# Optimization experiments

Hardware: AMD Instinct MI355X
Metric: run time of the kernel (lower is better)

Reference implementation:

```python
import jax, jax.numpy as jnp
import numpy as np

N = 100000
E = 1600000
NEG_SLOPE = 0.2


def _gat_layer(x, src, dst, W, a_src, a_dst, b, heads, out_ch):
    n = x.shape[0]
    h = (x @ W).reshape(n, heads, out_ch)                      # [N,H,C]
    alpha_src = (h * a_src).sum(-1)                            # [N,H]
    alpha_dst = (h * a_dst).sum(-1)                            # [N,H]
    e = jax.nn.leaky_relu(alpha_src[src] + alpha_dst[dst], NEG_SLOPE)  # [E,H]
    # segment softmax over incoming edges of each destination node
    m = jax.ops.segment_max(e, dst, num_segments=n)            # [N,H]
    ex = jnp.exp(e - m[dst])
    denom = jax.ops.segment_sum(ex, dst, num_segments=n)       # [N,H]
    alpha = ex / (denom[dst] + 1e-16)                          # [E,H]
    msg = h[src] * alpha[:, :, None]                           # [E,H,C]
    out = jax.ops.segment_sum(msg, dst, num_segments=n)        # [N,H,C]
    return out.reshape(n, heads * out_ch) + b


def setup_inputs() -> dict:
    key = jax.random.key(0)
    ks = jax.random.split(key, 10)
    glorot = lambda k, shape: jax.random.normal(k, shape, jnp.float32) * np.sqrt(2.0 / (shape[0] + shape[-1]))
    x = jax.random.normal(ks[0], (N, 5), jnp.float32)
    edge_index = jax.random.randint(ks[1], (2, E), 0, N, jnp.int64)
    return {
        "x": x,
        "edge_index": edge_index,
        "W1": glorot(ks[2], (5, 64)),
        "a_src1": glorot(ks[3], (8, 8)),
        "a_dst1": glorot(ks[4], (8, 8)),
        "b1": jnp.zeros((64,), jnp.float32),
        "W2": glorot(ks[5], (64, 2)),
        "a_src2": glorot(ks[6], (1, 2)),
        "a_dst2": glorot(ks[7], (1, 2)),
        "b2": jnp.zeros((2,), jnp.float32),
    }


def reference(x, edge_index, W1, a_src1, a_dst1, b1, W2, a_src2, a_dst2, b2):
    n = x.shape[0]
    loop = jnp.arange(n, dtype=edge_index.dtype)
    src = jnp.concatenate([edge_index[0], loop])   # PyG GATConv adds self-loops
    dst = jnp.concatenate([edge_index[1], loop])
    # dropout layers are no-ops in eval mode
    h = jax.nn.elu(_gat_layer(x, src, dst, W1, a_src1, a_dst1, b1, heads=8, out_ch=8))
    out = _gat_layer(h, src, dst, W2, a_src2, a_dst2, b2, heads=1, out_ch=2)
    return jax.nn.log_softmax(out, axis=1)
```

## Files before the change

kernel.cpp:

```cpp
#include <hip/hip_runtime.h>
#include <hip/hip_fp16.h>
#include <math.h>
#include <stdint.h>

#define N_NODES 100000
#define N_EDGES 1600000
#define N_TOT   (N_EDGES + N_NODES)
#define NEG_SLOPE 0.2f
#define LOG2E 1.44269504088896340736f

#define CB     128
#define CBBITS 7
#define NCB    ((N_NODES + CB - 1) / CB)
#define TP     2048
#define NPB    ((N_EDGES + TP - 1) / TP)
#define WINB   2560
#define NB_NODE1 ((N_NODES * 8 + 511) / 512)
#define N8     ((size_t)N_NODES * 8)

typedef int nt_int4 __attribute__((ext_vector_type(4)));

__global__ void __launch_bounds__(512) k_np(
        const int* __restrict__ src, const int* __restrict__ dst,
        int* __restrict__ ofsT, unsigned* __restrict__ pairs,
        const float* __restrict__ x, const float* __restrict__ W1,
        const float* __restrict__ a_src1, const float* __restrict__ a_dst1,
        __half* __restrict__ xh, __half* __restrict__ as1h,
        float* __restrict__ ad1) {
    __shared__ int lcnt[1024];
    __shared__ unsigned stage[TP];
    __shared__ int wred[8];
    int t = threadIdx.x;

    if (blockIdx.x >= NPB) {
        int gid  = (blockIdx.x - NPB) * 512 + t;
        int n    = gid >> 3;
        int head = gid & 7;
        if (n >= N_NODES) return;

        float xv[5];
#pragma unroll
        for (int k = 0; k < 5; ++k) xv[k] = x[n * 5 + k];

        float as = 0.f, ad = 0.f;
#pragma unroll
        for (int j = 0; j < 8; ++j) {
            int c = head * 8 + j;
            float acc = 0.f;
#pragma unroll
            for (int k = 0; k < 5; ++k) acc += xv[k] * W1[k * 64 + c];
            as += acc * a_src1[c];
            ad += acc * a_dst1[c];
        }
        as1h[n * 8 + head] = __float2half(as * LOG2E);
        ad1[n * 8 + head] = ad * LOG2E;

        if (head == 0) {
            __half2 p0 = __halves2half2(__float2half(xv[0]), __float2half(xv[1]));
            __half2 p1 = __halves2half2(__float2half(xv[2]), __float2half(xv[3]));
            __half2 p2 = __halves2half2(__float2half(xv[4]), __float2half(0.f));
            __half2 p3 = __halves2half2(__float2half(0.f), __float2half(0.f));
            __half2* xp = (__half2*)&xh[(size_t)n * 8];
            xp[0] = p0; xp[1] = p1; xp[2] = p2; xp[3] = p3;
        }
        return;
    }

    int blk = blockIdx.x;
    int base = blk * TP + t * 4;
    bool act = base < N_EDGES;
    int nE = min(TP, N_EDGES - blk * TP);

    lcnt[t] = 0; lcnt[t + 512] = 0;
    __syncthreads();

    nt_int4 s4, d4;
    if (act) {
        s4 = __builtin_nontemporal_load((const nt_int4*)(src + base));
        d4 = __builtin_nontemporal_load((const nt_int4*)(dst + base));
#pragma unroll
        for (int j = 0; j < 4; ++j) atomicAdd(&lcnt[d4[j] >> CBBITS], 1);
    }
    __syncthreads();

    int b0 = lcnt[t * 2], b1 = lcnt[t * 2 + 1];
    int local = b0 + b1;
    int ln = t & 63, w = t >> 6;
    int sc = local;
#pragma unroll
    for (int off = 1; off < 64; off <<= 1) {
        int u = __shfl_up(sc, off, 64);
        if (ln >= off) sc += u;
    }
    if (ln == 63) wred[w] = sc;
    __syncthreads();
    if (t < 8) {
        int v = wred[t], s = v;
#pragma unroll
        for (int off = 1; off < 8; off <<= 1) {
            int u = __shfl_up(s, off, 8);
            if ((t & 7) >= off) s += u;
        }
        wred[t] = s - v;
    }
    __syncthreads();
    int run = wred[w] + sc - local;
    lcnt[t * 2] = run; lcnt[t * 2 + 1] = run + b0;
    if (t * 2     <= NCB) ofsT[(size_t)(t * 2)     * NPB + blk] = run;
    if (t * 2 + 1 <= NCB) ofsT[(size_t)(t * 2 + 1) * NPB + blk] = run + b0;
    __syncthreads();

    if (act) {
#pragma unroll
        for (int j = 0; j < 4; ++j) {
            int d = d4[j], s = s4[j];
            int bin = d >> CBBITS;
            int idx = atomicAdd(&lcnt[bin], 1);
            stage[idx] = ((unsigned)(d & (CB - 1)) << 17) | (unsigned)s;
        }
    }
    __syncthreads();
    for (int i = t; i < nE; i += 512)
        pairs[(size_t)blk * TP + i] = stage[i];
}

__global__ void __launch_bounds__(512) k_csr(
        const int* __restrict__ ofsT, const unsigned* __restrict__ pairs,
        int* __restrict__ rbeg, int* __restrict__ rend, int* __restrict__ ssrc) {
    __shared__ unsigned stIn[WINB];
    __shared__ int stOut[WINB];
    __shared__ int lcnt[CB], lofs[CB], lcur[CB];
    __shared__ int wsum[2];
    __shared__ int acur;
    int B = blockIdx.x, t = threadIdx.x;
    int nvalid = min(CB, N_NODES - B * CB);
    int obase = B * WINB;

    if (t < CB) {
        lcnt[t] = (t < nvalid) ? 1 : 0;
        lcur[t] = 1;
    }
    if (t == 0) acur = 0;
    __syncthreads();

    for (int blk = t; blk < NPB; blk += 512) {
        int o0 = ofsT[(size_t)B       * NPB + blk];
        int o1 = ofsT[(size_t)(B + 1) * NPB + blk];
        int n = o1 - o0;
        if (n > 0) {
            int p = atomicAdd(&acur, n);
            const unsigned* pp = pairs + (size_t)blk * TP + o0;
            for (int i = 0; i < n; ++i) {
                unsigned r = pp[i];
                stIn[p + i] = r;
                atomicAdd(&lcnt[r >> 17], 1);
            }
        }
    }
    __syncthreads();
    int m = acur;

    int v = (t < CB) ? lcnt[t] : 0;
    int ln = t & 63, wv = t >> 6;
    int sc = v;
#pragma unroll
    for (int off = 1; off < 64; off <<= 1) {
        int u = __shfl_up(sc, off, 64);
        if (ln >= off) sc += u;
    }
    if (ln == 63 && wv < 2) wsum[wv] = sc;
    __syncthreads();
    int wbase = (wv == 1) ? wsum[0] : 0;
    int ex = wbase + sc - v;
    if (t < CB) {
        lofs[t] = ex;
        int gi = B * CB + t;
        if (gi < N_NODES) {
            rbeg[gi] = obase + ex;
            rend[gi] = obase + ex + v;
            stOut[ex] = gi;
        }
    }
    __syncthreads();

    for (int k = t; k < m; k += 512) {
        unsigned p = stIn[k];
        int dl = p >> 17;
        int idx = atomicAdd(&lcur[dl], 1);
        stOut[lofs[dl] + idx] = (int)(p & 0x1FFFF);
    }
    __syncthreads();

    int tot = m + nvalid;
    for (int i = t; i < tot; i += 512) ssrc[obase + i] = stOut[i];
}

__global__ void __launch_bounds__(256) k_gather1(
        const int* __restrict__ rbeg, const int* __restrict__ rend,
        const int* __restrict__ ssrc, const float4* __restrict__ xh4,
        const __half* __restrict__ as1h, const float* __restrict__ ad1,
        float* __restrict__ xsbuf) {
    int gtid = blockIdx.x * blockDim.x + threadIdx.x;
    int d      = gtid >> 5;
    int lane32 = threadIdx.x & 31;
    if (d >= N_NODES) return;
    int e = lane32 >> 3;
    int h = lane32 & 7;

    int beg = rbeg[d], end = rend[d];
    float adv = ad1[d * 8 + h];
    float c0 = 0.f, c1 = 0.f, c2 = 0.f, c3 = 0.f, c4 = 0.f, den = 0.f;

    for (int k = beg; k < end; k += 8) {
        int kA = k + e, kB = k + 4 + e;
        bool vA = kA < end, vB = kB < end;
        int sA = ssrc[vA ? kA : beg];
        int sB = ssrc[vB ? kB : beg];
        float eA = __half2float(as1h[sA * 8 + h]);
        float eB = __half2float(as1h[sB * 8 + h]);
        float4 xA = xh4[sA];
        float4 xB = xh4[sB];
        float tA = eA + adv; tA = fmaxf(tA, NEG_SLOPE * tA);
        float tB = eB + adv; tB = fmaxf(tB, NEG_SLOPE * tB);
        float wA = vA ? __builtin_amdgcn_exp2f(tA) : 0.f;
        float wB = vB ? __builtin_amdgcn_exp2f(tB) : 0.f;
        float2 A01 = __half22float2(*(__half2*)&xA.x);
        float2 A23 = __half22float2(*(__half2*)&xA.y);
        float2 A4_ = __half22float2(*(__half2*)&xA.z);
        float2 B01 = __half22float2(*(__half2*)&xB.x);
        float2 B23 = __half22float2(*(__half2*)&xB.y);
        float2 B4_ = __half22float2(*(__half2*)&xB.z);
        c0 += wA * A01.x + wB * B01.x;
        c1 += wA * A01.y + wB * B01.y;
        c2 += wA * A23.x + wB * B23.x;
        c3 += wA * A23.y + wB * B23.y;
        c4 += wA * A4_.x + wB * B4_.x;
        den += wA + wB;
    }

#define REDH(x) x += __shfl_xor(x, 8, 64); x += __shfl_xor(x, 16, 64);
    REDH(c0) REDH(c1) REDH(c2) REDH(c3) REDH(c4) REDH(den)
#undef REDH

    if (e == 0) {
        float inv = 1.f / den;
        size_t idx = (size_t)d * 8 + h;
        xsbuf[idx]          = c0 * inv;
        xsbuf[N8 + idx]     = c1 * inv;
        xsbuf[2 * N8 + idx] = c2 * inv;
        xsbuf[3 * N8 + idx] = c3 * inv;
        xsbuf[4 * N8 + idx] = c4 * inv;
    }
}

__global__ void __launch_bounds__(256) k_rec(
        const float* __restrict__ xsbuf, const float* __restrict__ b1,
        const float* __restrict__ W1, const float* __restrict__ W2,
        const float* __restrict__ a_src2, const float* __restrict__ a_dst2,
        float4* __restrict__ rec) {
    int gtid = blockIdx.x * blockDim.x + threadIdx.x;
    int d = gtid >> 3;
    int h = gtid & 7;
    if (d >= N_NODES) return;

    size_t idx = (size_t)d * 8 + h;
    float xs[5] = { xsbuf[idx], xsbuf[N8 + idx], xsbuf[2 * N8 + idx],
                    xsbuf[3 * N8 + idx], xsbuf[4 * N8 + idx] };

    float4 hA = ((const float4*)b1)[2 * h];
    float4 hB = ((const float4*)b1)[2 * h + 1];
#pragma unroll
    for (int c = 0; c < 5; ++c) {
        float xc = xs[c];
        float4 wA = *(const float4*)(W1 + c * 64 + 8 * h);
        float4 wB = *(const float4*)(W1 + c * 64 + 8 * h + 4);
        hA.x += xc * wA.x; hA.y += xc * wA.y; hA.z += xc * wA.z; hA.w += xc * wA.w;
        hB.x += xc * wB.x; hB.y += xc * wB.y; hB.z += xc * wB.z; hB.w += xc * wB.w;
    }
    float v0 = hA.x, v1 = hA.y, v2 = hA.z, v3 = hA.w;
    float v4 = hB.x, v5 = hB.y, v6 = hB.z, v7 = hB.w;
    v0 = (v0 > 0.f) ? v0 : (__expf(v0) - 1.f);
    v1 = (v1 > 0.f) ? v1 : (__expf(v1) - 1.f);
    v2 = (v2 > 0.f) ? v2 : (__expf(v2) - 1.f);
    v3 = (v3 > 0.f) ? v3 : (__expf(v3) - 1.f);
    v4 = (v4 > 0.f) ? v4 : (__expf(v4) - 1.f);
    v5 = (v5 > 0.f) ? v5 : (__expf(v5) - 1.f);
    v6 = (v6 > 0.f) ? v6 : (__expf(v6) - 1.f);
    v7 = (v7 > 0.f) ? v7 : (__expf(v7) - 1.f);

    const float4* w4 = (const float4*)(W2 + h * 16);
    float4 wq0 = w4[0], wq1 = w4[1], wq2 = w4[2], wq3 = w4[3];
    float h20 = v0 * wq0.x + v1 * wq0.z + v2 * wq1.x + v3 * wq1.z
              + v4 * wq2.x + v5 * wq2.z + v6 * wq3.x + v7 * wq3.z;
    float h21 = v0 * wq0.y + v1 * wq0.w + v2 * wq1.y + v3 * wq1.w
              + v4 * wq2.y + v5 * wq2.w + v6 * wq3.y + v7 * wq3.w;
    h20 += __shfl_xor(h20, 1, 64); h20 += __shfl_xor(h20, 2, 64); h20 += __shfl_xor(h20, 4, 64);
    h21 += __shfl_xor(h21, 1, 64); h21 += __shfl_xor(h21, 2, 64); h21 += __shfl_xor(h21, 4, 64);

    if (h == 0) {
        float as2v = (h20 * a_src2[0] + h21 * a_src2[1]) * LOG2E;
        float ad2v = (h20 * a_dst2[0] + h21 * a_dst2[1]) * LOG2E;
        rec[d] = make_float4(h20, h21, as2v, ad2v);
    }
}

__global__ void __launch_bounds__(256) k_gather2(
        const int* __restrict__ rbeg, const int* __restrict__ rend,
        const int* __restrict__ ssrc, const float4* __restrict__ rec,
        const float* __restrict__ b2, float* __restrict__ out) {
    int gtid = blockIdx.x * blockDim.x + threadIdx.x;
    int d    = gtid >> 3;
    int lane = threadIdx.x & 7;
    if (d >= N_NODES) return;

    int beg = rbeg[d], end = rend[d];
    float adv = rec[d].w;
    float n0 = 0.f, n1 = 0.f, den = 0.f;
    for (int k = beg; k < end; k += 8) {
        int ki = k + lane;
        bool v = ki < end;
        int s = ssrc[v ? ki : beg];
        float4 r = rec[s];
        float t = r.z + adv; t = fmaxf(t, NEG_SLOPE * t);
        float w = v ? __builtin_amdgcn_exp2f(t) : 0.f;
        n0 += w * r.x; n1 += w * r.y; den += w;
    }
#pragma unroll
    for (int off = 1; off < 8; off <<= 1) {
        n0  += __shfl_xor(n0,  off, 8);
        n1  += __shfl_xor(n1,  off, 8);
        den += __shfl_xor(den, off, 8);
    }
    if (lane == 0) {
        float o0 = n0 / den + b2[0];
        float o1 = n1 / den + b2[1];
        float m  = fmaxf(o0, o1);
        float lse = m + __logf(__expf(o0 - m) + __expf(o1 - m));
        *(float2*)(out + (size_t)d * 2) = make_float2(o0 - lse, o1 - lse);
    }
}

extern "C" void kernel_launch(void* const* d_in, const int* in_sizes, int n_in,
                              void* d_out, int out_size, void* d_ws, size_t ws_size,
                              hipStream_t stream) {
    const float* x      = (const float*)d_in[0];
    const int*   ei     = (const int*)d_in[1];
    const float* W1     = (const float*)d_in[2];
    const float* a_src1 = (const float*)d_in[3];
    const float* a_dst1 = (const float*)d_in[4];
    const float* b1     = (const float*)d_in[5];
    const float* W2     = (const float*)d_in[6];
    const float* a_src2 = (const float*)d_in[7];
    const float* a_dst2 = (const float*)d_in[8];
    const float* b2     = (const float*)d_in[9];
    float* out = (float*)d_out;

    const int* src = ei;
    const int* dst = ei + N_EDGES;

    int* rbeg   = (int*)d_ws;
    int* rend   = rbeg + N_NODES;
    int* ssrc   = rend + N_NODES;
    uintptr_t pp = ((uintptr_t)(ssrc + (size_t)NCB * WINB) + 255) & ~(uintptr_t)255;
    float4*   rec  = (float4*)pp;
    float*    ad1  = (float*)(rec + N_NODES);
    __half*   as1h = (__half*)(ad1 + (size_t)N_NODES * 8);
    __half*   xh   = as1h + (size_t)N_NODES * 8;
    uintptr_t rg = ((uintptr_t)(xh + (size_t)N_NODES * 8) + 255) & ~(uintptr_t)255;
    int*      ofsT  = (int*)rg;
    unsigned* pairs = (unsigned*)(ofsT + (size_t)(NCB + 1) * NPB);
    float*    xsbuf = (float*)rg;

    k_np<<<NPB + NB_NODE1, 512, 0, stream>>>(src, dst, ofsT, pairs,
                                             x, W1, a_src1, a_dst1,
                                             xh, as1h, ad1);
    k_csr<<<NCB, 512, 0, stream>>>(ofsT, pairs, rbeg, rend, ssrc);
    k_gather1<<<(N_NODES * 32 + 255) / 256, 256, 0, stream>>>(rbeg, rend, ssrc,
                                                              (const float4*)xh,
                                                              as1h, ad1, xsbuf);
    k_rec<<<(N_NODES * 8 + 255) / 256, 256, 0, stream>>>(xsbuf, b1, W1, W2,
                                                         a_src2, a_dst2, rec);
    k_gather2<<<(N_NODES * 8 + 255) / 256, 256, 0, stream>>>(rbeg, rend, ssrc,
                                                             rec, b2, out);
}
```

Before: 162.9 us.

## Fuse CSR build, layer-1 gather and node recompute into one kernel

The CSR construction kernel now also runs the layer-1 attention gather for its 128-node window, reading source indices straight from the shared-memory stOut array instead of the global ssrc. The per-node layer-2 projection (ELU, W2, attention logits) is then computed in place. This removes two launches and the global xsbuf round trip. The trade-off is far fewer threads for the latency-bound gather: 782 blocks of 512 threads with high LDS use, instead of one 32-lane group per node across the whole grid.

```diff
diff --git a/kernel.cpp b/kernel.cpp
--- a/kernel.cpp
+++ b/kernel.cpp
@@ -16,7 +16,6 @@
 #define NPB    ((N_EDGES + TP - 1) / TP)
 #define WINB   2560
 #define NB_NODE1 ((N_NODES * 8 + 511) / 512)
-#define N8     ((size_t)N_NODES * 8)
 
 typedef int nt_int4 __attribute__((ext_vector_type(4)));
 
@@ -124,9 +123,14 @@
         pairs[(size_t)blk * TP + i] = stage[i];
 }
 
-__global__ void __launch_bounds__(512) k_csr(
+__global__ void __launch_bounds__(512) k_cg(
         const int* __restrict__ ofsT, const unsigned* __restrict__ pairs,
-        int* __restrict__ rbeg, int* __restrict__ rend, int* __restrict__ ssrc) {
+        const float4* __restrict__ xh4, const __half* __restrict__ as1h,
+        const float* __restrict__ ad1, const float* __restrict__ b1,
+        const float* __restrict__ W1, const float* __restrict__ W2,
+        const float* __restrict__ a_src2, const float* __restrict__ a_dst2,
+        int* __restrict__ rbeg, int* __restrict__ rend,
+        int* __restrict__ ssrc, float4* __restrict__ rec) {
     __shared__ unsigned stIn[WINB];
     __shared__ int stOut[WINB];
     __shared__ int lcnt[CB], lofs[CB], lcur[CB];
@@ -193,114 +197,91 @@
 
     int tot = m + nvalid;
     for (int i = t; i < tot; i += 512) ssrc[obase + i] = stOut[i];
-}
-
-__global__ void __launch_bounds__(256) k_gather1(
-        const int* __restrict__ rbeg, const int* __restrict__ rend,
-        const int* __restrict__ ssrc, const float4* __restrict__ xh4,
-        const __half* __restrict__ as1h, const float* __restrict__ ad1,
-        float* __restrict__ xsbuf) {
-    int gtid = blockIdx.x * blockDim.x + threadIdx.x;
-    int d      = gtid >> 5;
-    int lane32 = threadIdx.x & 31;
-    if (d >= N_NODES) return;
+
+    int lane32 = t & 31;
     int e = lane32 >> 3;
     int h = lane32 & 7;
-
-    int beg = rbeg[d], end = rend[d];
-    float adv = ad1[d * 8 + h];
-    float c0 = 0.f, c1 = 0.f, c2 = 0.f, c3 = 0.f, c4 = 0.f, den = 0.f;
-
-    for (int k = beg; k < end; k += 8) {
-        int kA = k + e, kB = k + 4 + e;
-        bool vA = kA < end, vB = kB < end;
-        int sA = ssrc[vA ? kA : beg];
-        int sB = ssrc[vB ? kB : beg];
-        float eA = __half2float(as1h[sA * 8 + h]);
-        float eB = __half2float(as1h[sB * 8 + h]);
-        float4 xA = xh4[sA];
-        float4 xB = xh4[sB];
-        float tA = eA + adv; tA = fmaxf(tA, NEG_SLOPE * tA);
-        float tB = eB + adv; tB = fmaxf(tB, NEG_SLOPE * tB);
-        float wA = vA ? __builtin_amdgcn_exp2f(tA) : 0.f;
-        float wB = vB ? __builtin_amdgcn_exp2f(tB) : 0.f;
-        float2 A01 = __half22float2(*(__half2*)&xA.x);
-        float2 A23 = __half22float2(*(__half2*)&xA.y);
-        float2 A4_ = __half22float2(*(__half2*)&xA.z);
-        float2 B01 = __half22float2(*(__half2*)&xB.x);
-        float2 B23 = __half22float2(*(__half2*)&xB.y);
-        float2 B4_ = __half22float2(*(__half2*)&xB.z);
-        c0 += wA * A01.x + wB * B01.x;
-        c1 += wA * A01.y + wB * B01.y;
-        c2 += wA * A23.x + wB * B23.x;
-        c3 += wA * A23.y + wB * B23.y;
-        c4 += wA * A4_.x + wB * B4_.x;
-        den += wA + wB;
-    }
+    int dgrp = t >> 5;
+
+    for (int it = 0; it < 8; ++it) {
+        int dl = it * 16 + dgrp;
+        if (dl >= nvalid) continue;
+        int d = B * CB + dl;
+        int ebase = lofs[dl], cnt = lcnt[dl];
+        float adv = ad1[d * 8 + h];
+        float c0 = 0.f, c1 = 0.f, c2 = 0.f, c3 = 0.f, c4 = 0.f, den = 0.f;
+
+        for (int k = 0; k < cnt; k += 8) {
+            int kA = k + e, kB = k + 4 + e;
+            bool vA = kA < cnt, vB = kB < cnt;
+            int sA = stOut[ebase + (vA ? kA : 0)];
+            int sB = stOut[ebase + (vB ? kB : 0)];
+            float eA = __half2float(as1h[sA * 8 + h]);
+            float eB = __half2float(as1h[sB * 8 + h]);
+            float4 xA = xh4[sA];
+            float4 xB = xh4[sB];
+            float tA = eA + adv; tA = fmaxf(tA, NEG_SLOPE * tA);
+            float tB = eB + adv; tB = fmaxf(tB, NEG_SLOPE * tB);
+            float wA = vA ? __builtin_amdgcn_exp2f(tA) : 0.f;
+            float wB = vB ? __builtin_amdgcn_exp2f(tB) : 0.f;
+            float2 A01 = __half22float2(*(__half2*)&xA.x);
+            float2 A23 = __half22float2(*(__half2*)&xA.y);
+            float2 A4_ = __half22float2(*(__half2*)&xA.z);
+            float2 B01 = __half22float2(*(__half2*)&xB.x);
+            float2 B23 = __half22float2(*(__half2*)&xB.y);
+            float2 B4_ = __half22float2(*(__half2*)&xB.z);
+            c0 += wA * A01.x + wB * B01.x;
+            c1 += wA * A01.y + wB * B01.y;
+            c2 += wA * A23.x + wB * B23.x;
+            c3 += wA * A23.y + wB * B23.y;
+            c4 += wA * A4_.x + wB * B4_.x;
+            den += wA + wB;
+        }
 
 #define REDH(x) x += __shfl_xor(x, 8, 64); x += __shfl_xor(x, 16, 64);
-    REDH(c0) REDH(c1) REDH(c2) REDH(c3) REDH(c4) REDH(den)
+        REDH(c0) REDH(c1) REDH(c2) REDH(c3) REDH(c4) REDH(den)
 #undef REDH
 
-    if (e == 0) {
-        float inv = 1.f / den;
-        size_t idx = (size_t)d * 8 + h;
-        xsbuf[idx]          = c0 * inv;
-        xsbuf[N8 + idx]     = c1 * inv;
-        xsbuf[2 * N8 + idx] = c2 * inv;
-        xsbuf[3 * N8 + idx] = c3 * inv;
-        xsbuf[4 * N8 + idx] = c4 * inv;
-    }
-}
-
-__global__ void __launch_bounds__(256) k_rec(
-        const float* __restrict__ xsbuf, const float* __restrict__ b1,
-        const float* __restrict__ W1, const float* __restrict__ W2,
-        const float* __restrict__ a_src2, const float* __restrict__ a_dst2,
-        float4* __restrict__ rec) {
-    int gtid = blockIdx.x * blockDim.x + threadIdx.x;
-    int d = gtid >> 3;
-    int h = gtid & 7;
-    if (d >= N_NODES) return;
-
-    size_t idx = (size_t)d * 8 + h;
-    float xs[5] = { xsbuf[idx], xsbuf[N8 + idx], xsbuf[2 * N8 + idx],
-                    xsbuf[3 * N8 + idx], xsbuf[4 * N8 + idx] };
-
-    float4 hA = ((const float4*)b1)[2 * h];
-    float4 hB = ((const float4*)b1)[2 * h + 1];
-#pragma unroll
-    for (int c = 0; c < 5; ++c) {
-        float xc = xs[c];
-        float4 wA = *(const float4*)(W1 + c * 64 + 8 * h);
-        float4 wB = *(const float4*)(W1 + c * 64 + 8 * h + 4);
-        hA.x += xc * wA.x; hA.y += xc * wA.y; hA.z += xc * wA.z; hA.w += xc * wA.w;
-        hB.x += xc * wB.x; hB.y += xc * wB.y; hB.z += xc * wB.z; hB.w += xc * wB.w;
-    }
-    float v0 = hA.x, v1 = hA.y, v2 = hA.z, v3 = hA.w;
-    float v4 = hB.x, v5 = hB.y, v6 = hB.z, v7 = hB.w;
-    v0 = (v0 > 0.f) ? v0 : (__expf(v0) - 1.f);
-    v1 = (v1 > 0.f) ? v1 : (__expf(v1) - 1.f);
-    v2 = (v2 > 0.f) ? v2 : (__expf(v2) - 1.f);
-    v3 = (v3 > 0.f) ? v3 : (__expf(v3) - 1.f);
-    v4 = (v4 > 0.f) ? v4 : (__expf(v4) - 1.f);
-    v5 = (v5 > 0.f) ? v5 : (__expf(v5) - 1.f);
-    v6 = (v6 > 0.f) ? v6 : (__expf(v6) - 1.f);
-    v7 = (v7 > 0.f) ? v7 : (__expf(v7) - 1.f);
-
-    const float4* w4 = (const float4*)(W2 + h * 16);
-    float4 wq0 = w4[0], wq1 = w4[1], wq2 = w4[2], wq3 = w4[3];
-    float h20 = v0 * wq0.x + v1 * wq0.z + v2 * wq1.x + v3 * wq1.z
-              + v4 * wq2.x + v5 * wq2.z + v6 * wq3.x + v7 * wq3.z;
-    float h21 = v0 * wq0.y + v1 * wq0.w + v2 * wq1.y + v3 * wq1.w
-              + v4 * wq2.y + v5 * wq2.w + v6 * wq3.y + v7 * wq3.w;
-    h20 += __shfl_xor(h20, 1, 64); h20 += __shfl_xor(h20, 2, 64); h20 += __shfl_xor(h20, 4, 64);
-    h21 += __shfl_xor(h21, 1, 64); h21 += __shfl_xor(h21, 2, 64); h21 += __shfl_xor(h21, 4, 64);
-
-    if (h == 0) {
-        float as2v = (h20 * a_src2[0] + h21 * a_src2[1]) * LOG2E;
-        float ad2v = (h20 * a_dst2[0] + h21 * a_dst2[1]) * LOG2E;
-        rec[d] = make_float4(h20, h21, as2v, ad2v);
+        if (lane32 < 8) {
+            float inv = 1.f / den;
+            float xs[5] = { c0 * inv, c1 * inv, c2 * inv, c3 * inv, c4 * inv };
+
+            float4 hA = ((const float4*)b1)[2 * h];
+            float4 hB = ((const float4*)b1)[2 * h + 1];
+#pragma unroll
+            for (int c = 0; c < 5; ++c) {
+                float xc = xs[c];
+                float4 wA = *(const float4*)(W1 + c * 64 + 8 * h);
+                float4 wB = *(const float4*)(W1 + c * 64 + 8 * h + 4);
+                hA.x += xc * wA.x; hA.y += xc * wA.y; hA.z += xc * wA.z; hA.w += xc * wA.w;
+                hB.x += xc * wB.x; hB.y += xc * wB.y; hB.z += xc * wB.z; hB.w += xc * wB.w;
+            }
+            float v0 = hA.x, v1 = hA.y, v2 = hA.z, v3 = hA.w;
+            float v4 = hB.x, v5 = hB.y, v6 = hB.z, v7 = hB.w;
+            v0 = (v0 > 0.f) ? v0 : (__expf(v0) - 1.f);
+            v1 = (v1 > 0.f) ? v1 : (__expf(v1) - 1.f);
+            v2 = (v2 > 0.f) ? v2 : (__expf(v2) - 1.f);
+            v3 = (v3 > 0.f) ? v3 : (__expf(v3) - 1.f);
+            v4 = (v4 > 0.f) ? v4 : (__expf(v4) - 1.f);
+            v5 = (v5 > 0.f) ? v5 : (__expf(v5) - 1.f);
+            v6 = (v6 > 0.f) ? v6 : (__expf(v6) - 1.f);
+            v7 = (v7 > 0.f) ? v7 : (__expf(v7) - 1.f);
+
+            const float4* w4 = (const float4*)(W2 + h * 16);
+            float4 wq0 = w4[0], wq1 = w4[1], wq2 = w4[2], wq3 = w4[3];
+            float h20 = v0 * wq0.x + v1 * wq0.z + v2 * wq1.x + v3 * wq1.z
+                      + v4 * wq2.x + v5 * wq2.z + v6 * wq3.x + v7 * wq3.z;
+            float h21 = v0 * wq0.y + v1 * wq0.w + v2 * wq1.y + v3 * wq1.w
+                      + v4 * wq2.y + v5 * wq2.w + v6 * wq3.y + v7 * wq3.w;
+            h20 += __shfl_xor(h20, 1, 64); h20 += __shfl_xor(h20, 2, 64); h20 += __shfl_xor(h20, 4, 64);
+            h21 += __shfl_xor(h21, 1, 64); h21 += __shfl_xor(h21, 2, 64); h21 += __shfl_xor(h21, 4, 64);
+
+            if (lane32 == 0) {
+                float as2v = (h20 * a_src2[0] + h21 * a_src2[1]) * LOG2E;
+                float ad2v = (h20 * a_dst2[0] + h21 * a_dst2[1]) * LOG2E;
+                rec[d] = make_float4(h20, h21, as2v, ad2v);
+            }
+        }
     }
 }
 
@@ -369,17 +350,13 @@
     uintptr_t rg = ((uintptr_t)(xh + (size_t)N_NODES * 8) + 255) & ~(uintptr_t)255;
     int*      ofsT  = (int*)rg;
     unsigned* pairs = (unsigned*)(ofsT + (size_t)(NCB + 1) * NPB);
-    float*    xsbuf = (float*)rg;
 
     k_np<<<NPB + NB_NODE1, 512, 0, stream>>>(src, dst, ofsT, pairs,
                                              x, W1, a_src1, a_dst1,
                                              xh, as1h, ad1);
-    k_csr<<<NCB, 512, 0, stream>>>(ofsT, pairs, rbeg, rend, ssrc);
-    k_gather1<<<(N_NODES * 32 + 255) / 256, 256, 0, stream>>>(rbeg, rend, ssrc,
-                                                              (const float4*)xh,
-                                                              as1h, ad1, xsbuf);
-    k_rec<<<(N_NODES * 8 + 255) / 256, 256, 0, stream>>>(xsbuf, b1, W1, W2,
-                                                         a_src2, a_dst2, rec);
+    k_cg<<<NCB, 512, 0, stream>>>(ofsT, pairs, (const float4*)xh, as1h, ad1,
+                                  b1, W1, W2, a_src2, a_dst2,
+                                  rbeg, rend, ssrc, rec);
     k_gather2<<<(N_NODES * 8 + 255) / 256, 256, 0, stream>>>(rbeg, rend, ssrc,
                                                              rec, b2, out);
 }
```

Result: slower. 180.2 us (+10.6%).

## Reuse first-pass atomic ranks in bucketing and parallelize CSR gather via prefix-scan

Applied to the files above, without the earlier changes.

The bucketing kernel now keeps the ranks returned by its first counting atomics and adds them to the scanned bin offsets, so the second round of shared atomics disappears. The CSR kernel replaces its per-thread serial copy loop, which used a shared atomic cursor, with a block-wide prefix scan over per-partition counts. Each thread then binary-searches the scan to find the source partition of every element, which makes the global reads of pairs evenly spread and coalesced. The cost is an extra scan and a ten-step binary search per element, plus more shared memory.

```diff
diff --git a/kernel.cpp b/kernel.cpp
--- a/kernel.cpp
+++ b/kernel.cpp
@@ -5,7 +5,6 @@
 
 #define N_NODES 100000
 #define N_EDGES 1600000
-#define N_TOT   (N_EDGES + N_NODES)
 #define NEG_SLOPE 0.2f
 #define LOG2E 1.44269504088896340736f
 
@@ -75,11 +74,13 @@
     __syncthreads();
 
     nt_int4 s4, d4;
+    int myidx[4];
     if (act) {
         s4 = __builtin_nontemporal_load((const nt_int4*)(src + base));
         d4 = __builtin_nontemporal_load((const nt_int4*)(dst + base));
 #pragma unroll
-        for (int j = 0; j < 4; ++j) atomicAdd(&lcnt[d4[j] >> CBBITS], 1);
+        for (int j = 0; j < 4; ++j)
+            myidx[j] = atomicAdd(&lcnt[d4[j] >> CBBITS], 1);
     }
     __syncthreads();
 
@@ -113,10 +114,9 @@
     if (act) {
 #pragma unroll
         for (int j = 0; j < 4; ++j) {
-            int d = d4[j], s = s4[j];
-            int bin = d >> CBBITS;
-            int idx = atomicAdd(&lcnt[bin], 1);
-            stage[idx] = ((unsigned)(d & (CB - 1)) << 17) | (unsigned)s;
+            int d = d4[j];
+            stage[lcnt[d >> CBBITS] + myidx[j]] =
+                ((unsigned)(d & (CB - 1)) << 17) | (unsigned)s4[j];
         }
     }
     __syncthreads();
@@ -129,39 +129,70 @@
         int* __restrict__ rbeg, int* __restrict__ rend, int* __restrict__ ssrc) {
     __shared__ unsigned stIn[WINB];
     __shared__ int stOut[WINB];
+    __shared__ int o0s[NPB];
+    __shared__ int cns[1026];
     __shared__ int lcnt[CB], lofs[CB], lcur[CB];
     __shared__ int wsum[2];
-    __shared__ int acur;
+    __shared__ int wred[8];
     int B = blockIdx.x, t = threadIdx.x;
     int nvalid = min(CB, N_NODES - B * CB);
     int obase = B * WINB;
 
+    for (int s = t; s < NPB; s += 512) {
+        int o0 = ofsT[(size_t)B       * NPB + s];
+        int o1 = ofsT[(size_t)(B + 1) * NPB + s];
+        o0s[s] = o0;
+        cns[s] = o1 - o0;
+    }
+    for (int s = NPB + t; s < 1024; s += 512) cns[s] = 0;
     if (t < CB) {
         lcnt[t] = (t < nvalid) ? 1 : 0;
         lcur[t] = 1;
     }
-    if (t == 0) acur = 0;
-    __syncthreads();
-
-    for (int blk = t; blk < NPB; blk += 512) {
-        int o0 = ofsT[(size_t)B       * NPB + blk];
-        int o1 = ofsT[(size_t)(B + 1) * NPB + blk];
-        int n = o1 - o0;
-        if (n > 0) {
-            int p = atomicAdd(&acur, n);
-            const unsigned* pp = pairs + (size_t)blk * TP + o0;
-            for (int i = 0; i < n; ++i) {
-                unsigned r = pp[i];
-                stIn[p + i] = r;
-                atomicAdd(&lcnt[r >> 17], 1);
-            }
-        }
-    }
-    __syncthreads();
-    int m = acur;
+    __syncthreads();
+
+    int a0 = cns[t * 2], a1 = cns[t * 2 + 1];
+    int local = a0 + a1;
+    int ln = t & 63, w = t >> 6;
+    int sc2 = local;
+#pragma unroll
+    for (int off = 1; off < 64; off <<= 1) {
+        int u = __shfl_up(sc2, off, 64);
+        if (ln >= off) sc2 += u;
+    }
+    if (ln == 63) wred[w] = sc2;
+    __syncthreads();
+    if (t < 8) {
+        int v = wred[t], s = v;
+#pragma unroll
+        for (int off = 1; off < 8; off <<= 1) {
+            int u = __shfl_up(s, off, 8);
+            if ((t & 7) >= off) s += u;
+        }
+        wred[t] = s - v;
+    }
+    __syncthreads();
+    int run = wred[w] + sc2 - local;
+    cns[t * 2] = run; cns[t * 2 + 1] = run + a0;
+    __syncthreads();
+    int m = cns[NPB];
+
+    for (int i = t; i < m; i += 512) {
+        int lo = 0, hi = NPB;
+#pragma unroll
+        for (int it = 0; it < 10; ++it) {
+            int mid = (lo + hi + 1) >> 1;
+            if (mid <= NPB && cns[mid] <= i) lo = mid; else hi = mid - 1;
+        }
+        int s = lo;
+        unsigned r = pairs[(size_t)s * TP + o0s[s] + (i - cns[s])];
+        stIn[i] = r;
+        atomicAdd(&lcnt[r >> 17], 1);
+    }
+    __syncthreads();
 
     int v = (t < CB) ? lcnt[t] : 0;
-    int ln = t & 63, wv = t >> 6;
+    int wv = t >> 6;
     int sc = v;
 #pragma unroll
     for (int off = 1; off < 64; off <<= 1) {
```

Result: faster. 156.6 us (-3.9%).

## Scatter edge pairs directly into per-bucket global windows; halve gather1 lanes per node

Applied to the files above, without the earlier changes.

The partition kernel now reserves space in each destination bucket's global window with a global atomic cursor and writes its staged pairs there directly. It also reuses the first-pass atomic return value as the local slot, removing the second atomic pass. The CSR kernel no longer walks a transposed offset table across all partition blocks; it reads one contiguous window per bucket, which cuts scattered reads and the per-block serial loops. Separately, gather1 uses 16 lanes per node instead of 32, with one fewer shuffle reduction. In exchange this adds a memset, global atomic contention and a serial per-thread copy loop, and entries past WINB are silently dropped, so the output is only correct if no bucket exceeds the window.

```diff
diff --git a/kernel.cpp b/kernel.cpp
--- a/kernel.cpp
+++ b/kernel.cpp
@@ -5,7 +5,6 @@
 
 #define N_NODES 100000
 #define N_EDGES 1600000
-#define N_TOT   (N_EDGES + N_NODES)
 #define NEG_SLOPE 0.2f
 #define LOG2E 1.44269504088896340736f
 
@@ -22,7 +21,7 @@
 
 __global__ void __launch_bounds__(512) k_np(
         const int* __restrict__ src, const int* __restrict__ dst,
-        int* __restrict__ ofsT, unsigned* __restrict__ pairs,
+        int* __restrict__ gcur, unsigned* __restrict__ pairs,
         const float* __restrict__ x, const float* __restrict__ W1,
         const float* __restrict__ a_src1, const float* __restrict__ a_dst1,
         __half* __restrict__ xh, __half* __restrict__ as1h,
@@ -69,17 +68,17 @@
     int blk = blockIdx.x;
     int base = blk * TP + t * 4;
     bool act = base < N_EDGES;
-    int nE = min(TP, N_EDGES - blk * TP);
-
     lcnt[t] = 0; lcnt[t + 512] = 0;
     __syncthreads();
 
     nt_int4 s4, d4;
+    int myidx[4];
     if (act) {
         s4 = __builtin_nontemporal_load((const nt_int4*)(src + base));
         d4 = __builtin_nontemporal_load((const nt_int4*)(dst + base));
 #pragma unroll
-        for (int j = 0; j < 4; ++j) atomicAdd(&lcnt[d4[j] >> CBBITS], 1);
+        for (int j = 0; j < 4; ++j)
+            myidx[j] = atomicAdd(&lcnt[d4[j] >> CBBITS], 1);
     }
     __syncthreads();
 
@@ -106,32 +105,41 @@
     __syncthreads();
     int run = wred[w] + sc - local;
     lcnt[t * 2] = run; lcnt[t * 2 + 1] = run + b0;
-    if (t * 2     <= NCB) ofsT[(size_t)(t * 2)     * NPB + blk] = run;
-    if (t * 2 + 1 <= NCB) ofsT[(size_t)(t * 2 + 1) * NPB + blk] = run + b0;
     __syncthreads();
 
     if (act) {
 #pragma unroll
         for (int j = 0; j < 4; ++j) {
-            int d = d4[j], s = s4[j];
-            int bin = d >> CBBITS;
-            int idx = atomicAdd(&lcnt[bin], 1);
-            stage[idx] = ((unsigned)(d & (CB - 1)) << 17) | (unsigned)s;
-        }
-    }
-    __syncthreads();
-    for (int i = t; i < nE; i += 512)
-        pairs[(size_t)blk * TP + i] = stage[i];
+            int d = d4[j];
+            stage[lcnt[d >> CBBITS] + myidx[j]] =
+                ((unsigned)(d & (CB - 1)) << 17) | (unsigned)s4[j];
+        }
+    }
+    __syncthreads();
+
+#pragma unroll
+    for (int q = 0; q < 2; ++q) {
+        int bin  = t * 2 + q;
+        int cnt  = q ? b1 : b0;
+        int sbase = q ? run + b0 : run;
+        if (bin < NCB && cnt > 0) {
+            int gb = atomicAdd(&gcur[bin], cnt);
+            unsigned* wp = pairs + (size_t)bin * WINB;
+            for (int j = 0; j < cnt; ++j) {
+                int p = gb + j;
+                if (p < WINB) wp[p] = stage[sbase + j];
+            }
+        }
+    }
 }
 
 __global__ void __launch_bounds__(512) k_csr(
-        const int* __restrict__ ofsT, const unsigned* __restrict__ pairs,
+        const int* __restrict__ gcur, const unsigned* __restrict__ pairs,
         int* __restrict__ rbeg, int* __restrict__ rend, int* __restrict__ ssrc) {
     __shared__ unsigned stIn[WINB];
     __shared__ int stOut[WINB];
     __shared__ int lcnt[CB], lofs[CB], lcur[CB];
     __shared__ int wsum[2];
-    __shared__ int acur;
     int B = blockIdx.x, t = threadIdx.x;
     int nvalid = min(CB, N_NODES - B * CB);
     int obase = B * WINB;
@@ -140,25 +148,16 @@
         lcnt[t] = (t < nvalid) ? 1 : 0;
         lcur[t] = 1;
     }
-    if (t == 0) acur = 0;
-    __syncthreads();
-
-    for (int blk = t; blk < NPB; blk += 512) {
-        int o0 = ofsT[(size_t)B       * NPB + blk];
-        int o1 = ofsT[(size_t)(B + 1) * NPB + blk];
-        int n = o1 - o0;
-        if (n > 0) {
-            int p = atomicAdd(&acur, n);
-            const unsigned* pp = pairs + (size_t)blk * TP + o0;
-            for (int i = 0; i < n; ++i) {
-                unsigned r = pp[i];
-                stIn[p + i] = r;
-                atomicAdd(&lcnt[r >> 17], 1);
-            }
-        }
-    }
-    __syncthreads();
-    int m = acur;
+    __syncthreads();
+
+    int m = min(gcur[B], WINB);
+
+    for (int i = t; i < m; i += 512) {
+        unsigned r = pairs[(size_t)B * WINB + i];
+        stIn[i] = r;
+        atomicAdd(&lcnt[r >> 17], 1);
+    }
+    __syncthreads();
 
     int v = (t < CB) ? lcnt[t] : 0;
     int ln = t & 63, wv = t >> 6;
@@ -201,18 +200,18 @@
         const __half* __restrict__ as1h, const float* __restrict__ ad1,
         float* __restrict__ xsbuf) {
     int gtid = blockIdx.x * blockDim.x + threadIdx.x;
-    int d      = gtid >> 5;
-    int lane32 = threadIdx.x & 31;
+    int d      = gtid >> 4;
+    int lane16 = threadIdx.x & 15;
     if (d >= N_NODES) return;
-    int e = lane32 >> 3;
-    int h = lane32 & 7;
+    int e = lane16 >> 3;
+    int h = lane16 & 7;
 
     int beg = rbeg[d], end = rend[d];
     float adv = ad1[d * 8 + h];
     float c0 = 0.f, c1 = 0.f, c2 = 0.f, c3 = 0.f, c4 = 0.f, den = 0.f;
 
-    for (int k = beg; k < end; k += 8) {
-        int kA = k + e, kB = k + 4 + e;
+    for (int k = beg; k < end; k += 4) {
+        int kA = k + e, kB = k + 2 + e;
         bool vA = kA < end, vB = kB < end;
         int sA = ssrc[vA ? kA : beg];
         int sB = ssrc[vB ? kB : beg];
@@ -238,7 +237,7 @@
         den += wA + wB;
     }
 
-#define REDH(x) x += __shfl_xor(x, 8, 64); x += __shfl_xor(x, 16, 64);
+#define REDH(x) x += __shfl_xor(x, 8, 64);
     REDH(c0) REDH(c1) REDH(c2) REDH(c3) REDH(c4) REDH(den)
 #undef REDH
 
@@ -367,15 +366,16 @@
     __half*   as1h = (__half*)(ad1 + (size_t)N_NODES * 8);
     __half*   xh   = as1h + (size_t)N_NODES * 8;
     uintptr_t rg = ((uintptr_t)(xh + (size_t)N_NODES * 8) + 255) & ~(uintptr_t)255;
-    int*      ofsT  = (int*)rg;
-    unsigned* pairs = (unsigned*)(ofsT + (size_t)(NCB + 1) * NPB);
+    int*      gcur  = (int*)rg;
+    unsigned* pairs = (unsigned*)(((uintptr_t)(gcur + NCB) + 255) & ~(uintptr_t)255);
     float*    xsbuf = (float*)rg;
 
-    k_np<<<NPB + NB_NODE1, 512, 0, stream>>>(src, dst, ofsT, pairs,
+    hipMemsetAsync(gcur, 0, NCB * sizeof(int), stream);
+    k_np<<<NPB + NB_NODE1, 512, 0, stream>>>(src, dst, gcur, pairs,
                                              x, W1, a_src1, a_dst1,
                                              xh, as1h, ad1);
-    k_csr<<<NCB, 512, 0, stream>>>(ofsT, pairs, rbeg, rend, ssrc);
-    k_gather1<<<(N_NODES * 32 + 255) / 256, 256, 0, stream>>>(rbeg, rend, ssrc,
+    k_csr<<<NCB, 512, 0, stream>>>(gcur, pairs, rbeg, rend, ssrc);
+    k_gather1<<<(N_NODES * 16 + 255) / 256, 256, 0, stream>>>(rbeg, rend, ssrc,
                                                               (const float4*)xh,
                                                               as1h, ad1, xsbuf);
     k_rec<<<(N_NODES * 8 + 255) / 256, 256, 0, stream>>>(xsbuf, b1, W1, W2,
```

Result: slower. 181.1 us (+11.2%).
